# Kernel optimization log

Measured on AMD Instinct MI355X. Metric: run time of the kernel, lower is better.

The kernel has to match this reference:

```python
import jax, jax.numpy as jnp
import numpy as np

GROUPS = 32
EPS = 1e-5


def _group_norm(x, w, b):
    B, C, H, W = x.shape
    xr = x.reshape(B, GROUPS, C // GROUPS, H, W)
    mean = xr.mean(axis=(2, 3, 4), keepdims=True)
    var = xr.var(axis=(2, 3, 4), keepdims=True)
    xn = ((xr - mean) * jax.lax.rsqrt(var + EPS)).reshape(B, C, H, W)
    return xn * w[None, :, None, None] + b[None, :, None, None]


def _conv1x1(w, b, x):
    # 1x1 conv == per-pixel channel matmul
    return jnp.einsum('oc,bchw->bohw', w, x) + b[None, :, None, None]


def setup_inputs() -> dict:
    key = jax.random.key(0)
    ks = jax.random.split(key, 6)
    C = 512
    s = 1.0 / np.sqrt(C)  # kaiming-uniform-ish scale for 1x1 convs
    return {
        'x': jax.random.normal(ks[0], (4, C, 64, 64), jnp.float32),
        'gn_w': jnp.ones((C,), jnp.float32),
        'gn_b': jnp.zeros((C,), jnp.float32),
        'qw': jax.random.normal(ks[1], (C, C), jnp.float32) * s,
        'qb': jnp.zeros((C,), jnp.float32),
        'kw': jax.random.normal(ks[2], (C, C), jnp.float32) * s,
        'kb': jnp.zeros((C,), jnp.float32),
        'vw': jax.random.normal(ks[3], (C, C), jnp.float32) * s,
        'vb': jnp.zeros((C,), jnp.float32),
        'pw': jax.random.normal(ks[4], (C, C), jnp.float32) * s,
        'pb': jnp.zeros((C,), jnp.float32),
    }


def reference(x, gn_w, gn_b, qw, qb, kw, kb, vw, vb, pw, pb):
    B, C, H, W = x.shape
    h_ = _group_norm(x, gn_w, gn_b)
    q = _conv1x1(qw, qb, h_).reshape(B, C, H * W)
    k = _conv1x1(kw, kb, h_).reshape(B, C, H * W)
    v = _conv1x1(vw, vb, h_).reshape(B, C, H * W)
    # scores [B, HW(query), HW(key)]
    scores = jnp.einsum('bcq,bck->bqk', q, k) * (C ** -0.5)
    attn = jax.nn.softmax(scores, axis=-1)
    out = jnp.einsum('bqk,bdk->bdq', attn, v).reshape(B, C, H, W)
    return x + _conv1x1(pw, pb, out)
```

## Files before the change

### kernel.cpp

```cpp
#include <hip/hip_runtime.h>

#define DEV __device__ __forceinline__

typedef __attribute__((ext_vector_type(8))) short short8;
typedef __attribute__((ext_vector_type(4))) float floatx4;
typedef __attribute__((ext_vector_type(4))) int i32x4;
typedef __attribute__((ext_vector_type(2))) long longx2;

DEV unsigned short f2bs(float x) {
    unsigned u = __float_as_uint(x);
    unsigned r = (u + 0x7fffu + ((u >> 16) & 1u)) >> 16;
    return (unsigned short)r;
}

DEV unsigned char f2fp8(float x) {
#if __has_builtin(__builtin_amdgcn_cvt_pk_fp8_f32)
    int pk = __builtin_amdgcn_cvt_pk_fp8_f32(x, 0.f, 0, false);
    return (unsigned char)(pk & 0xff);
#else
    unsigned u = __float_as_uint(x);
    unsigned s = (u >> 24) & 0x80;
    unsigned a = u & 0x7fffffff;
    unsigned um = a + 0x7ffffu + ((a >> 20) & 1u);
    unsigned r = (a >= 0x3c800000u) ? ((um >> 20) - 0x3C0u) : 0u;
    return (unsigned char)(r | s);
#endif
}

DEV unsigned pack_fp8x4(float v0, float v1, float v2, float v3) {
#if __has_builtin(__builtin_amdgcn_cvt_pk_fp8_f32)
    unsigned pk = (unsigned)__builtin_amdgcn_cvt_pk_fp8_f32(v0, v1, 0, false);
    pk = (unsigned)__builtin_amdgcn_cvt_pk_fp8_f32(v2, v3, (int)pk, true);
    return pk;
#else
    return (unsigned)f2fp8(v0) | ((unsigned)f2fp8(v1) << 8) |
           ((unsigned)f2fp8(v2) << 16) | ((unsigned)f2fp8(v3) << 24);
#endif
}

DEV unsigned pack_i8x4(float v0, float v1, float v2, float v3) {
    unsigned b0 = (unsigned)((int)rintf(v0)) & 255u;
    unsigned b1 = (unsigned)((int)rintf(v1)) & 255u;
    unsigned b2 = (unsigned)((int)rintf(v2)) & 255u;
    unsigned b3 = (unsigned)((int)rintf(v3)) & 255u;
    return b0 | (b1 << 8) | (b2 << 16) | (b3 << 24);
}

DEV void syncfull() {
    asm volatile("s_waitcnt vmcnt(0) lgkmcnt(0)" ::: "memory");
    __builtin_amdgcn_sched_barrier(0);
    __builtin_amdgcn_s_barrier();
    __builtin_amdgcn_sched_barrier(0);
}

__global__ void pre_kernel(const float* __restrict__ x,
                           const float* __restrict__ qw, const float* __restrict__ kw,
                           const float* __restrict__ vw, const float* __restrict__ pw,
                           const float* __restrict__ qb, const float* __restrict__ kb,
                           unsigned short* __restrict__ wqkb, unsigned short* __restrict__ wvb,
                           unsigned short* __restrict__ wpb,
                           float* __restrict__ biasqk,
                           float* __restrict__ stats) {
    int b = blockIdx.x, tid = threadIdx.x;
    if (b < 768) {
        const float* src = (b < 256) ? qw : (b < 512) ? kw : vw;
        unsigned short* dst = (b < 256) ? wqkb : (b < 512) ? (wqkb + 262144) : wvb;
        int off = (b & 255) * 256 + tid;
        float4 v = ((const float4*)src)[off];
        ushort4 o;
        o.x = f2bs(v.x); o.y = f2bs(v.y); o.z = f2bs(v.z); o.w = f2bs(v.w);
        ((ushort4*)dst)[off] = o;
    } else if (b < 1024) {
        int off = (b - 768) * 256 + tid;
        int row = off >> 7, c4 = (off & 127) * 4;
        float4 v = ((const float4*)pw)[off];
        float vv[4] = {v.x, v.y, v.z, v.w};
#pragma unroll
        for (int e = 0; e < 4; ++e) {
            int c = c4 + e;
            int j = (c >> 4) & 3, lc = c & 15;
            int cp = (c & ~63) | (lc * 4 + j);
            wpb[row * 512 + cp] = f2bs(vv[e]);
        }
    } else if (b == 1024) {
        biasqk[tid]       = qb[tid];
        biasqk[256 + tid] = qb[256 + tid];
        biasqk[512 + tid] = kb[tid];
        biasqk[768 + tid] = kb[256 + tid];
    } else {
        int bg = b - 1025;
        const float4* p = (const float4*)(x + (size_t)bg * 65536);
        float s = 0.f, ss = 0.f;
        for (int i = tid; i < 16384; i += 256) {
            float4 v = p[i];
            s += v.x + v.y + v.z + v.w;
            ss += v.x * v.x + v.y * v.y + v.z * v.z + v.w * v.w;
        }
        for (int off = 32; off; off >>= 1) { s += __shfl_down(s, off); ss += __shfl_down(ss, off); }
        __shared__ float rs[4], rss[4];
        int wave = tid >> 6, lane = tid & 63;
        if (lane == 0) { rs[wave] = s; rss[wave] = ss; }
        __syncthreads();
        if (tid == 0) {
            float S = rs[0] + rs[1] + rs[2] + rs[3];
            float SS = rss[0] + rss[1] + rss[2] + rss[3];
            float mean = S * (1.f / 65536.f);
            float var = SS * (1.f / 65536.f) - mean * mean;
            stats[bg * 2] = mean;
            stats[bg * 2 + 1] = rsqrtf(var + 1e-5f);
        }
    }
}

__global__ void gn_apply_kernel(const float* __restrict__ x, const float* __restrict__ stats,
                                const float* __restrict__ gw, const float* __restrict__ gb,
                                unsigned short* __restrict__ ht) {
    __shared__ __align__(16) unsigned short t[64][72];
    int b = blockIdx.z, c0 = blockIdx.y * 64, p0 = blockIdx.x * 64;
    int tid = threadIdx.x;
    const float* xb = x + ((size_t)b * 512 + c0) * 4096 + p0;
#pragma unroll
    for (int pass = 0; pass < 4; ++pass) {
        int cl = pass * 16 + (tid >> 4);
        int pq = (tid & 15) * 4;
        float4 v = *(const float4*)(xb + (size_t)cl * 4096 + pq);
        int c = c0 + cl, g = c >> 4;
        float mean = stats[(b * 32 + g) * 2], rstd = stats[(b * 32 + g) * 2 + 1];
        float sw = gw[c] * rstd;
        float sb = gb[c] - mean * sw;
        t[pq + 0][cl] = f2bs(v.x * sw + sb);
        t[pq + 1][cl] = f2bs(v.y * sw + sb);
        t[pq + 2][cl] = f2bs(v.z * sw + sb);
        t[pq + 3][cl] = f2bs(v.w * sw + sb);
    }
    __syncthreads();
    unsigned short* hb = ht + ((size_t)b * 4096 + p0) * 512 + c0;
#pragma unroll
    for (int pass = 0; pass < 2; ++pass) {
        int pl = pass * 32 + (tid >> 3);
        int c8 = (tid & 7) * 8;
        *(uint4*)(hb + (size_t)pl * 512 + c8) = *(const uint4*)&t[pl][c8];
    }
}

__global__ void gemm_qkv(const unsigned short* __restrict__ h_t, long long sP,
                         const unsigned short* __restrict__ wqkb,
                         const unsigned short* __restrict__ wvb,
                         char* __restrict__ q_i8, char* __restrict__ k_i8,
                         char* __restrict__ v_f8,
                         const float* __restrict__ biasqk, const float* __restrict__ vb,
                         float qs) {
    __shared__ __align__(16) unsigned short lA[128 * 64];
    __shared__ __align__(16) unsigned short lB[128 * 64];
    const int tid = threadIdx.x;
    const int wave = tid >> 6, lane = tid & 63;
    const int flat = blockIdx.x;
    const bool isqk = flat < 1024;
    int m0, n0, bz;
    const unsigned short *Ab, *Bb;
    if (isqk) {
        m0 = ((flat >> 3) & 31) * 128;
        n0 = (flat & 7) * 128;
        bz = flat >> 8;
        Ab = h_t + (size_t)bz * sP;
        Bb = wqkb;
    } else {
        const int g = flat - 1024;
        m0 = ((g >> 5) & 3) * 128;
        n0 = (g & 31) * 128;
        bz = g >> 7;
        Ab = wvb;
        Bb = h_t + (size_t)bz * sP;
    }

    floatx4 acc[4][4];
#pragma unroll
    for (int i = 0; i < 4; i++)
#pragma unroll
        for (int j = 0; j < 4; j++) acc[i][j] = (floatx4){0.f, 0.f, 0.f, 0.f};

    const int wm = (wave >> 1) * 64, wn = (wave & 1) * 64;
    const int quad = lane >> 4;
    const int lc = lane & 15;
    const int lc7 = lc & 7;

    for (int kt = 0; kt < 8; ++kt) {
        const int kbase = kt * 64;
#pragma unroll
        for (int c = 0; c < 4; ++c) {
            int d = c * 256 + tid;
            int r = d >> 3;
            int kc = (d & 7) ^ (r & 7);
            const unsigned short* ga = Ab + (size_t)(m0 + r) * 512 + kbase + kc * 8;
            const unsigned short* gb = Bb + (size_t)(n0 + r) * 512 + kbase + kc * 8;
            __builtin_amdgcn_global_load_lds(
                (const __attribute__((address_space(1))) void*)ga,
                (__attribute__((address_space(3))) void*)&lA[(size_t)(c * 256 + wave * 64) * 8], 16, 0, 0);
            __builtin_amdgcn_global_load_lds(
                (const __attribute__((address_space(1))) void*)gb,
                (__attribute__((address_space(3))) void*)&lB[(size_t)(c * 256 + wave * 64) * 8], 16, 0, 0);
        }
        __syncthreads();
#pragma unroll
        for (int kk = 0; kk < 2; ++kk) {
            const int swz = ((kk * 4 + quad) ^ lc7) * 8;
            short8 af[4], bf[4];
#pragma unroll
            for (int i = 0; i < 4; i++)
                af[i] = *(const short8*)&lA[(size_t)(wm + i * 16 + lc) * 64 + swz];
#pragma unroll
            for (int j = 0; j < 4; j++)
                bf[j] = *(const short8*)&lB[(size_t)(wn + j * 16 + lc) * 64 + swz];
#pragma unroll
            for (int i = 0; i < 4; i++)
#pragma unroll
                for (int j = 0; j < 4; j++)
                    acc[i][j] = __builtin_amdgcn_mfma_f32_16x16x32_bf16(af[i], bf[j], acc[i][j], 0, 0, 0);
        }
        __syncthreads();
    }

    const int rowb = quad * 4;
    if (isqk) {
#pragma unroll
        for (int i = 0; i < 4; i++) {
#pragma unroll
            for (int r = 0; r < 4; r++) {
                const int m = m0 + wm + i * 16 + rowb + r;
                float q[4];
#pragma unroll
                for (int j = 0; j < 4; j++) {
                    const int n = n0 + wn + j * 16 + lc;
                    q[j] = fminf(fmaxf((acc[i][j][r] + biasqk[n]) * qs, -127.f), 127.f);
                }
                const int col64 = n0 + wn;
                char* outp = (col64 < 512) ? q_i8 : k_i8;
                size_t idx = (size_t)bz * sP + (size_t)m * 512 +
                             (col64 - ((col64 < 512) ? 0 : 512)) + lc * 4;
                *(unsigned*)(outp + idx) = pack_i8x4(q[0], q[1], q[2], q[3]);
            }
        }
    } else {
#pragma unroll
        for (int i = 0; i < 4; i++) {
#pragma unroll
            for (int r = 0; r < 4; r++) {
                const int m = m0 + wm + i * 16 + rowb + r;
                const float bm = vb[m];
                float q[4];
#pragma unroll
                for (int j = 0; j < 4; j++)
                    q[j] = fminf(fmaxf(acc[i][j][r] + bm, -448.f), 448.f);
                size_t idx = (size_t)bz * sP + (size_t)m * 4096 + n0 + wn + lc * 4;
                *(unsigned*)(v_f8 + idx) = pack_fp8x4(q[0], q[1], q[2], q[3]);
            }
        }
    }
}

__global__ __launch_bounds__(512, 2) void attn_fused(
    const char* __restrict__ Qg, const char* __restrict__ Kg,
    const char* __restrict__ Vg,
    unsigned short* __restrict__ Ou, long long sOb,
    float* __restrict__ rsum, float scale2) {
    __shared__ __align__(16) char Ql[128 * 512];
    __shared__ __align__(16) char Kl[64 * 512];
    __shared__ __align__(16) char Vl[512 * 64];
    __shared__ __align__(16) char Pl[128 * 64];
    const int tid = threadIdx.x;
    const int wave = tid >> 6, lane = tid & 63;
    const int quad = lane >> 4, lc = lane & 15;
    const int id = blockIdx.x;
    const int xcd = id & 7, qi = id >> 3;
    const int bz = xcd >> 1, split = xcd & 1;
    const int q0 = qi * 128;
    const int kvbase = split * 2048;
    const int NIT = 32;

    const char* Qb = Qg + ((size_t)bz * 4096 + q0) * 512;
    const char* Kb = Kg + ((size_t)bz * 4096 + kvbase) * 512;
    const char* Vb = Vg + (size_t)bz * 2097152 + kvbase;

    const int wq = wave * 16;
    const int mO = (wave >> 2) * 64, nO = (wave & 3) * 128;

    auto stageQ = [&]() {
#pragma unroll
        for (int c = 0; c < 8; ++c) {
            int f = c * 512 + tid;
            int r = f >> 5, g = f & 31;
            int gs = (g & 24) | ((g & 7) ^ (r & 7));
            __builtin_amdgcn_global_load_lds(
                (const __attribute__((address_space(1))) void*)(Qb + (size_t)r * 512 + gs * 16),
                (__attribute__((address_space(3))) void*)(Ql + (size_t)f * 16), 16, 0, 0);
        }
    };
    auto stageK = [&](int t) {
#pragma unroll
        for (int c = 0; c < 4; ++c) {
            int f = c * 512 + tid;
            int r = f >> 5, g = f & 31;
            int gs = (g & 24) | ((g & 7) ^ (r & 7));
            __builtin_amdgcn_global_load_lds(
                (const __attribute__((address_space(1))) void*)(Kb + (size_t)(t * 64 + r) * 512 + gs * 16),
                (__attribute__((address_space(3))) void*)(Kl + (size_t)f * 16), 16, 0, 0);
        }
    };
    auto stageV = [&](int t) {
#pragma unroll
        for (int c = 0; c < 4; ++c) {
            int f = c * 512 + tid;
            int r = f >> 2, g = f & 3;
            int gs = g ^ (r & 3);
            __builtin_amdgcn_global_load_lds(
                (const __attribute__((address_space(1))) void*)(Vb + (size_t)r * 4096 + t * 64 + gs * 16),
                (__attribute__((address_space(3))) void*)(Vl + (size_t)f * 16), 16, 0, 0);
        }
    };

    floatx4 acco[4][8];
#pragma unroll
    for (int i = 0; i < 4; ++i)
#pragma unroll
        for (int j = 0; j < 8; ++j) acco[i][j] = (floatx4){0.f, 0.f, 0.f, 0.f};
    float rs = 0.f;

    stageQ();
    stageK(0);
    stageV(0);
    syncfull();

    const int q = wq + lc;
    const int q7 = q & 7;

    for (int t = 0; t < NIT; ++t) {
        if (t > 0) stageV(t);
        i32x4 accs[4];
#pragma unroll
        for (int ki = 0; ki < 4; ++ki) accs[ki] = (i32x4){0, 0, 0, 0};
#pragma unroll
        for (int ks = 0; ks < 8; ++ks) {
            const int g = ks * 4 + quad;
            i32x4 bfrag = *(const i32x4*)&Ql[(size_t)q * 512 +
                                             (((g & 24) | ((g & 7) ^ q7)) << 4)];
#pragma unroll
            for (int ki = 0; ki < 4; ++ki) {
                const int ar = ki * 16 + lc;
                i32x4 afrag = *(const i32x4*)&Kl[(size_t)ar * 512 +
                                                 (((g & 24) | ((g & 7) ^ (ar & 7))) << 4)];
                accs[ki] = __builtin_amdgcn_mfma_i32_16x16x64_i8(afrag, bfrag, accs[ki], 0, 0, 0);
            }
        }
        float e[4][4];
#pragma unroll
        for (int ki = 0; ki < 4; ++ki)
#pragma unroll
            for (int r = 0; r < 4; ++r) {
                e[ki][r] = fminf(exp2f(fmaf((float)accs[ki][r], scale2, -2.0f)), 448.f);
                rs += e[ki][r];
            }
#pragma unroll
        for (int r = 0; r < 4; ++r) {
            unsigned w = pack_fp8x4(e[0][r], e[1][r], e[2][r], e[3][r]);
            const int s4 = quad * 4 + r;
            const int byte = q * 64 + (((s4 >> 1) ^ q7) << 3) + ((s4 & 1) << 2);
            *(unsigned*)&Pl[byte] = w;
        }
        syncfull();

        if (t + 1 < NIT) stageK(t + 1);
#pragma unroll
        for (int ks2 = 0; ks2 < 2; ++ks2) {
            long pa[4], vf[8];
#pragma unroll
            for (int i = 0; i < 4; ++i) {
                const int row = mO + i * 16 + lc;
                pa[i] = *(const long*)&Pl[(size_t)row * 64 +
                                          (((ks2 * 4 + quad) ^ (row & 7)) << 3)];
            }
#pragma unroll
            for (int j = 0; j < 8; ++j) {
                const int row = nO + j * 16 + lc;
                const int g16 = ks2 * 2 + (quad >> 1);
                vf[j] = *(const long*)&Vl[(size_t)row * 64 +
                                          ((g16 ^ (row & 3)) << 4) + ((quad & 1) << 3)];
            }
#pragma unroll
            for (int i = 0; i < 4; ++i)
#pragma unroll
                for (int j = 0; j < 8; ++j)
                    acco[i][j] = __builtin_amdgcn_mfma_f32_16x16x32_fp8_fp8(pa[i], vf[j], acco[i][j], 0, 0, 0);
        }
        syncfull();
    }

    rs += __shfl_xor(rs, 16);
    rs += __shfl_xor(rs, 32);
    if (quad == 0) rsum[((size_t)(split * 4 + bz)) * 4096 + q0 + q] = rs;

#pragma unroll
    for (int i = 0; i < 4; ++i) {
#pragma unroll
        for (int r = 0; r < 4; ++r) {
            const int m = q0 + mO + i * 16 + quad * 4 + r;
            unsigned short h[8];
#pragma unroll
            for (int j = 0; j < 8; ++j) h[j] = f2bs(acco[i][j][r]);
            unsigned short* base = Ou + (size_t)bz * sOb + (size_t)m * 1024 + split * 512 + nO;
            uint2 u0, u1;
            u0.x = (unsigned)h[0] | ((unsigned)h[1] << 16);
            u0.y = (unsigned)h[2] | ((unsigned)h[3] << 16);
            u1.x = (unsigned)h[4] | ((unsigned)h[5] << 16);
            u1.y = (unsigned)h[6] | ((unsigned)h[7] << 16);
            *(uint2*)(base + lc * 4) = u0;
            *(uint2*)(base + 64 + lc * 4) = u1;
        }
    }
}

__global__ void gemm_proj(const unsigned short* __restrict__ A,
                          const unsigned short* __restrict__ B, long long sBb,
                          float* __restrict__ Cv, long long sCb,
                          const float* __restrict__ bias,
                          const float* __restrict__ resid, long long sRb,
                          const float* __restrict__ rsum,
                          int M, int N, int K) {
    __shared__ __align__(16) unsigned short lA[128 * 64];
    __shared__ __align__(16) unsigned short lB[128 * 64];
    const int tid = threadIdx.x;
    const int wave = tid >> 6, lane = tid & 63;
    const int m0 = blockIdx.y * 128, n0 = blockIdx.x * 128, bz = blockIdx.z;
    const unsigned short* Ab = A;
    const unsigned short* Bb = B + (size_t)bz * sBb;

    floatx4 acc[4][4];
#pragma unroll
    for (int i = 0; i < 4; i++)
#pragma unroll
        for (int j = 0; j < 4; j++) acc[i][j] = (floatx4){0.f, 0.f, 0.f, 0.f};

    const int wm = (wave >> 1) * 64, wn = (wave & 1) * 64;
    const int quad = lane >> 4;
    const int lc = lane & 15;
    const int lc7 = lc & 7;

    const int nk = K >> 6;
    for (int kt = 0; kt < nk; ++kt) {
        const int kbase = kt * 64;
#pragma unroll
        for (int c = 0; c < 4; ++c) {
            int d = c * 256 + tid;
            int r = d >> 3;
            int kc = (d & 7) ^ (r & 7);
            const unsigned short* ga = Ab + (size_t)(m0 + r) * 512 + ((kbase & 511) + kc * 8);
            const unsigned short* gb = Bb + (size_t)(n0 + r) * 1024 + kbase + kc * 8;
            __builtin_amdgcn_global_load_lds(
                (const __attribute__((address_space(1))) void*)ga,
                (__attribute__((address_space(3))) void*)&lA[(size_t)(c * 256 + wave * 64) * 8], 16, 0, 0);
            __builtin_amdgcn_global_load_lds(
                (const __attribute__((address_space(1))) void*)gb,
                (__attribute__((address_space(3))) void*)&lB[(size_t)(c * 256 + wave * 64) * 8], 16, 0, 0);
        }
        __syncthreads();
#pragma unroll
        for (int kk = 0; kk < 2; ++kk) {
            const int swz = ((kk * 4 + quad) ^ lc7) * 8;
            short8 af[4], bf[4];
#pragma unroll
            for (int i = 0; i < 4; i++)
                af[i] = *(const short8*)&lA[(size_t)(wm + i * 16 + lc) * 64 + swz];
#pragma unroll
            for (int j = 0; j < 4; j++)
                bf[j] = *(const short8*)&lB[(size_t)(wn + j * 16 + lc) * 64 + swz];
#pragma unroll
            for (int i = 0; i < 4; i++)
#pragma unroll
                for (int j = 0; j < 4; j++)
                    acc[i][j] = __builtin_amdgcn_mfma_f32_16x16x32_bf16(af[i], bf[j], acc[i][j], 0, 0, 0);
        }
        __syncthreads();
    }

    float rsinv[4];
#pragma unroll
    for (int j = 0; j < 4; j++) {
        const int n = n0 + wn + j * 16 + lc;
        rsinv[j] = 1.f / (rsum[(size_t)bz * 4096 + n] + rsum[(size_t)(4 + bz) * 4096 + n]);
    }

    const int rowb = quad * 4;
#pragma unroll
    for (int i = 0; i < 4; i++) {
#pragma unroll
        for (int r = 0; r < 4; r++) {
            const int m = m0 + wm + i * 16 + rowb + r;
            const float bm = bias[m];
#pragma unroll
            for (int j = 0; j < 4; j++) {
                const int n = n0 + wn + j * 16 + lc;
                size_t idx = (size_t)bz * sCb + (size_t)m * N + n;
                Cv[idx] = acc[i][j][r] * rsinv[j] + bm + resid[(size_t)bz * sRb + (size_t)m * N + n];
            }
        }
    }
}

extern "C" void kernel_launch(void* const* d_in, const int* in_sizes, int n_in,
                              void* d_out, int out_size, void* d_ws, size_t ws_size,
                              hipStream_t stream) {
    (void)in_sizes; (void)n_in; (void)out_size; (void)ws_size;
    const float* x   = (const float*)d_in[0];
    const float* gnw = (const float*)d_in[1];
    const float* gnb = (const float*)d_in[2];
    const float* qw  = (const float*)d_in[3];
    const float* qb  = (const float*)d_in[4];
    const float* kw  = (const float*)d_in[5];
    const float* kb  = (const float*)d_in[6];
    const float* vw  = (const float*)d_in[7];
    const float* vb  = (const float*)d_in[8];
    const float* pw  = (const float*)d_in[9];
    const float* pb  = (const float*)d_in[10];
    float* out = (float*)d_out;

    char* ws = (char*)d_ws;
    unsigned short* h_t = (unsigned short*)(ws);
    char* q_i8 = (char*)(ws + (16ull << 20));
    char* k_i8 = (char*)(ws + (32ull << 20));
    char* v_f8 = (char*)(ws + (48ull << 20));
    unsigned short* wqkb = (unsigned short*)(ws + (64ull << 20));
    unsigned short* wvb = (unsigned short*)(ws + (65ull << 20));
    unsigned short* wpb = wvb + 262144;
    float* stats  = (float*)(ws + (66ull << 20));
    float* biasqk = (float*)(ws + (66ull << 20) + 8192);
    float* rowsum = (float*)(ws + (66ull << 20) + 65536);
    unsigned short* o_un = (unsigned short*)(ws + (72ull << 20));

    const long long sP  = 2097152;
    const long long sOb = 4194304;
    const float QS = 16.f;
    const float SC = 0.044194173824159216f / (QS * QS);
    const float LOG2E = 1.4426950408889634f;

    pre_kernel<<<1153, 256, 0, stream>>>(x, qw, kw, vw, pw, qb, kb, wqkb, wvb, wpb,
                                         biasqk, stats);
    gn_apply_kernel<<<dim3(64, 8, 4), 256, 0, stream>>>(x, stats, gnw, gnb, h_t);
    gemm_qkv<<<1536, 256, 0, stream>>>(h_t, sP, wqkb, wvb, q_i8, k_i8, v_f8, biasqk, vb, QS);
    attn_fused<<<dim3(256), 512, 0, stream>>>(q_i8, k_i8, v_f8, o_un, sOb, rowsum,
                                              SC * LOG2E);
    gemm_proj<<<dim3(32, 4, 4), 256, 0, stream>>>(wpb, o_un, sOb, out, sP, pb, x, sP,
                                                  rowsum, 512, 4096, 1024);
}
```

Baseline: 313.6 us.

## Re-layout attention LDS tiles for wide 16-byte fragment reads

Rewrites the shared-memory layouts of Q, K, V and P in the fused attention kernel. Q and K are stored in 128-byte channel chunks with XOR swizzle, and V is packed two channel rows per 128-byte LDS row. P uses an 80-byte padded row stride so the PV stage reads 16-byte fragments, halving the number of LDS reads, and issues the MFMAs in two passes over the pair. The goal is fewer LDS instructions and fewer bank conflicts in the inner loop. It adds complex index mapping that could introduce conflicts or correctness risk if the swizzles mismatch.

```diff
diff --git a/kernel.cpp b/kernel.cpp
--- a/kernel.cpp
+++ b/kernel.cpp
@@ -258,166 +258,6 @@
     }
 }
 
-__global__ __launch_bounds__(512, 2) void attn_fused(
-    const char* __restrict__ Qg, const char* __restrict__ Kg,
-    const char* __restrict__ Vg,
-    unsigned short* __restrict__ Ou, long long sOb,
-    float* __restrict__ rsum, float scale2) {
-    __shared__ __align__(16) char Ql[128 * 512];
-    __shared__ __align__(16) char Kl[64 * 512];
-    __shared__ __align__(16) char Vl[512 * 64];
-    __shared__ __align__(16) char Pl[128 * 64];
-    const int tid = threadIdx.x;
-    const int wave = tid >> 6, lane = tid & 63;
-    const int quad = lane >> 4, lc = lane & 15;
-    const int id = blockIdx.x;
-    const int xcd = id & 7, qi = id >> 3;
-    const int bz = xcd >> 1, split = xcd & 1;
-    const int q0 = qi * 128;
-    const int kvbase = split * 2048;
-    const int NIT = 32;
-
-    const char* Qb = Qg + ((size_t)bz * 4096 + q0) * 512;
-    const char* Kb = Kg + ((size_t)bz * 4096 + kvbase) * 512;
-    const char* Vb = Vg + (size_t)bz * 2097152 + kvbase;
-
-    const int wq = wave * 16;
-    const int mO = (wave >> 2) * 64, nO = (wave & 3) * 128;
-
-    auto stageQ = [&]() {
-#pragma unroll
-        for (int c = 0; c < 8; ++c) {
-            int f = c * 512 + tid;
-            int r = f >> 5, g = f & 31;
-            int gs = (g & 24) | ((g & 7) ^ (r & 7));
-            __builtin_amdgcn_global_load_lds(
-                (const __attribute__((address_space(1))) void*)(Qb + (size_t)r * 512 + gs * 16),
-                (__attribute__((address_space(3))) void*)(Ql + (size_t)f * 16), 16, 0, 0);
-        }
-    };
-    auto stageK = [&](int t) {
-#pragma unroll
-        for (int c = 0; c < 4; ++c) {
-            int f = c * 512 + tid;
-            int r = f >> 5, g = f & 31;
-            int gs = (g & 24) | ((g & 7) ^ (r & 7));
-            __builtin_amdgcn_global_load_lds(
-                (const __attribute__((address_space(1))) void*)(Kb + (size_t)(t * 64 + r) * 512 + gs * 16),
-                (__attribute__((address_space(3))) void*)(Kl + (size_t)f * 16), 16, 0, 0);
-        }
-    };
-    auto stageV = [&](int t) {
-#pragma unroll
-        for (int c = 0; c < 4; ++c) {
-            int f = c * 512 + tid;
-            int r = f >> 2, g = f & 3;
-            int gs = g ^ (r & 3);
-            __builtin_amdgcn_global_load_lds(
-                (const __attribute__((address_space(1))) void*)(Vb + (size_t)r * 4096 + t * 64 + gs * 16),
-                (__attribute__((address_space(3))) void*)(Vl + (size_t)f * 16), 16, 0, 0);
-        }
-    };
-
-    floatx4 acco[4][8];
-#pragma unroll
-    for (int i = 0; i < 4; ++i)
-#pragma unroll
-        for (int j = 0; j < 8; ++j) acco[i][j] = (floatx4){0.f, 0.f, 0.f, 0.f};
-    float rs = 0.f;
-
-    stageQ();
-    stageK(0);
-    stageV(0);
-    syncfull();
-
-    const int q = wq + lc;
-    const int q7 = q & 7;
-
-    for (int t = 0; t < NIT; ++t) {
-        if (t > 0) stageV(t);
-        i32x4 accs[4];
-#pragma unroll
-        for (int ki = 0; ki < 4; ++ki) accs[ki] = (i32x4){0, 0, 0, 0};
-#pragma unroll
-        for (int ks = 0; ks < 8; ++ks) {
-            const int g = ks * 4 + quad;
-            i32x4 bfrag = *(const i32x4*)&Ql[(size_t)q * 512 +
-                                             (((g & 24) | ((g & 7) ^ q7)) << 4)];
-#pragma unroll
-            for (int ki = 0; ki < 4; ++ki) {
-                const int ar = ki * 16 + lc;
-                i32x4 afrag = *(const i32x4*)&Kl[(size_t)ar * 512 +
-                                                 (((g & 24) | ((g & 7) ^ (ar & 7))) << 4)];
-                accs[ki] = __builtin_amdgcn_mfma_i32_16x16x64_i8(afrag, bfrag, accs[ki], 0, 0, 0);
-            }
-        }
-        float e[4][4];
-#pragma unroll
-        for (int ki = 0; ki < 4; ++ki)
-#pragma unroll
-            for (int r = 0; r < 4; ++r) {
-                e[ki][r] = fminf(exp2f(fmaf((float)accs[ki][r], scale2, -2.0f)), 448.f);
-                rs += e[ki][r];
-            }
-#pragma unroll
-        for (int r = 0; r < 4; ++r) {
-            unsigned w = pack_fp8x4(e[0][r], e[1][r], e[2][r], e[3][r]);
-            const int s4 = quad * 4 + r;
-            const int byte = q * 64 + (((s4 >> 1) ^ q7) << 3) + ((s4 & 1) << 2);
-            *(unsigned*)&Pl[byte] = w;
-        }
-        syncfull();
-
-        if (t + 1 < NIT) stageK(t + 1);
-#pragma unroll
-        for (int ks2 = 0; ks2 < 2; ++ks2) {
-            long pa[4], vf[8];
-#pragma unroll
-            for (int i = 0; i < 4; ++i) {
-                const int row = mO + i * 16 + lc;
-                pa[i] = *(const long*)&Pl[(size_t)row * 64 +
-                                          (((ks2 * 4 + quad) ^ (row & 7)) << 3)];
-            }
-#pragma unroll
-            for (int j = 0; j < 8; ++j) {
-                const int row = nO + j * 16 + lc;
-                const int g16 = ks2 * 2 + (quad >> 1);
-                vf[j] = *(const long*)&Vl[(size_t)row * 64 +
-                                          ((g16 ^ (row & 3)) << 4) + ((quad & 1) << 3)];
-            }
-#pragma unroll
-            for (int i = 0; i < 4; ++i)
-#pragma unroll
-                for (int j = 0; j < 8; ++j)
-                    acco[i][j] = __builtin_amdgcn_mfma_f32_16x16x32_fp8_fp8(pa[i], vf[j], acco[i][j], 0, 0, 0);
-        }
-        syncfull();
-    }
-
-    rs += __shfl_xor(rs, 16);
-    rs += __shfl_xor(rs, 32);
-    if (quad == 0) rsum[((size_t)(split * 4 + bz)) * 4096 + q0 + q] = rs;
-
-#pragma unroll
-    for (int i = 0; i < 4; ++i) {
-#pragma unroll
-        for (int r = 0; r < 4; ++r) {
-            const int m = q0 + mO + i * 16 + quad * 4 + r;
-            unsigned short h[8];
-#pragma unroll
-            for (int j = 0; j < 8; ++j) h[j] = f2bs(acco[i][j][r]);
-            unsigned short* base = Ou + (size_t)bz * sOb + (size_t)m * 1024 + split * 512 + nO;
-            uint2 u0, u1;
-            u0.x = (unsigned)h[0] | ((unsigned)h[1] << 16);
-            u0.y = (unsigned)h[2] | ((unsigned)h[3] << 16);
-            u1.x = (unsigned)h[4] | ((unsigned)h[5] << 16);
-            u1.y = (unsigned)h[6] | ((unsigned)h[7] << 16);
-            *(uint2*)(base + lc * 4) = u0;
-            *(uint2*)(base + 64 + lc * 4) = u1;
-        }
-    }
-}
-
 __global__ void gemm_proj(const unsigned short* __restrict__ A,
                           const unsigned short* __restrict__ B, long long sBb,
                           float* __restrict__ Cv, long long sCb,
@@ -501,6 +341,175 @@
                 size_t idx = (size_t)bz * sCb + (size_t)m * N + n;
                 Cv[idx] = acc[i][j][r] * rsinv[j] + bm + resid[(size_t)bz * sRb + (size_t)m * N + n];
             }
+        }
+    }
+}
+
+__global__ __launch_bounds__(512, 2) void attn_fused(
+    const char* __restrict__ Qg, const char* __restrict__ Kg,
+    const char* __restrict__ Vg,
+    unsigned short* __restrict__ Ou, long long sOb,
+    float* __restrict__ rsum, float scale2) {
+    __shared__ __align__(16) char Ql[512 * 128];
+    __shared__ __align__(16) char Kl[256 * 128];
+    __shared__ __align__(16) char Vl[256 * 128];
+    __shared__ __align__(16) char Pl[128 * 80];
+    const int tid = threadIdx.x;
+    const int wave = tid >> 6, lane = tid & 63;
+    const int quad = lane >> 4, lc = lane & 15;
+    const int lc7 = lc & 7;
+    const int id = blockIdx.x;
+    const int xcd = id & 7, qi = id >> 3;
+    const int bz = xcd >> 1, split = xcd & 1;
+    const int q0 = qi * 128;
+    const int kvbase = split * 2048;
+    const int NIT = 32;
+
+    const char* Qb = Qg + ((size_t)bz * 4096 + q0) * 512;
+    const char* Kb = Kg + ((size_t)bz * 4096 + kvbase) * 512;
+    const char* Vb = Vg + (size_t)bz * 2097152 + kvbase;
+
+    const int wq = wave * 16;
+    const int mO = (wave >> 2) * 64, nO = (wave & 3) * 128;
+
+    auto stageQ = [&]() {
+#pragma unroll
+        for (int c = 0; c < 8; ++c) {
+            int f = c * 512 + tid;
+            int rr = f >> 3, cs = f & 7;
+            int qq = rr & 127, chq = rr >> 7;
+            int s = cs ^ (qq & 7);
+            __builtin_amdgcn_global_load_lds(
+                (const __attribute__((address_space(1))) void*)(Qb + (size_t)qq * 512 + chq * 128 + s * 16),
+                (__attribute__((address_space(3))) void*)(Ql + (size_t)f * 16), 16, 0, 0);
+        }
+    };
+    auto stageK = [&](int t) {
+#pragma unroll
+        for (int c = 0; c < 4; ++c) {
+            int f = c * 512 + tid;
+            int rr = f >> 3, cs = f & 7;
+            int kv = rr & 63, chq = rr >> 6;
+            int s = cs ^ (kv & 7);
+            __builtin_amdgcn_global_load_lds(
+                (const __attribute__((address_space(1))) void*)(Kb + (size_t)(t * 64 + kv) * 512 + chq * 128 + s * 16),
+                (__attribute__((address_space(3))) void*)(Kl + (size_t)f * 16), 16, 0, 0);
+        }
+    };
+    auto stageV = [&](int t) {
+#pragma unroll
+        for (int c = 0; c < 4; ++c) {
+            int f = c * 512 + tid;
+            int rr = f >> 3, cs = f & 7;
+            int cp = cs ^ (rr & 7);
+            int d = rr + ((cp >> 2) << 8);
+            int gq = cp & 3;
+            __builtin_amdgcn_global_load_lds(
+                (const __attribute__((address_space(1))) void*)(Vb + (size_t)d * 4096 + t * 64 + gq * 16),
+                (__attribute__((address_space(3))) void*)(Vl + (size_t)f * 16), 16, 0, 0);
+        }
+    };
+
+    floatx4 acco[4][8];
+#pragma unroll
+    for (int i = 0; i < 4; ++i)
+#pragma unroll
+        for (int j = 0; j < 8; ++j) acco[i][j] = (floatx4){0.f, 0.f, 0.f, 0.f};
+    float rs = 0.f;
+
+    stageQ();
+    stageK(0);
+    stageV(0);
+    syncfull();
+
+    const int q = wq + lc;
+    const int q7 = q & 7;
+
+    for (int t = 0; t < NIT; ++t) {
+        if (t > 0) stageV(t);
+        i32x4 accs[4];
+#pragma unroll
+        for (int ki = 0; ki < 4; ++ki) accs[ki] = (i32x4){0, 0, 0, 0};
+#pragma unroll
+        for (int ks = 0; ks < 8; ++ks) {
+            const int g = ks * 4 + quad;
+            const int gh = g >> 3, gl = g & 7;
+            i32x4 bfrag = *(const i32x4*)&Ql[(size_t)(gh * 128 + q) * 128 + ((gl ^ q7) << 4)];
+#pragma unroll
+            for (int ki = 0; ki < 4; ++ki) {
+                const int ar = ki * 16 + lc;
+                i32x4 afrag = *(const i32x4*)&Kl[(size_t)(gh * 64 + ar) * 128 + ((gl ^ lc7) << 4)];
+                accs[ki] = __builtin_amdgcn_mfma_i32_16x16x64_i8(afrag, bfrag, accs[ki], 0, 0, 0);
+            }
+        }
+        float e[4][4];
+#pragma unroll
+        for (int ki = 0; ki < 4; ++ki)
+#pragma unroll
+            for (int r = 0; r < 4; ++r) {
+                e[ki][r] = fminf(exp2f(fmaf((float)accs[ki][r], scale2, -2.0f)), 448.f);
+                rs += e[ki][r];
+            }
+        {
+            unsigned w0 = pack_fp8x4(e[0][0], e[1][0], e[2][0], e[3][0]);
+            unsigned w1 = pack_fp8x4(e[0][1], e[1][1], e[2][1], e[3][1]);
+            unsigned w2 = pack_fp8x4(e[0][2], e[1][2], e[2][2], e[3][2]);
+            unsigned w3 = pack_fp8x4(e[0][3], e[1][3], e[2][3], e[3][3]);
+            uint2 s0; s0.x = w0; s0.y = w1;
+            uint2 s1; s1.x = w2; s1.y = w3;
+            *(uint2*)&Pl[(size_t)q * 80 + quad * 16 + 0] = s0;
+            *(uint2*)&Pl[(size_t)q * 80 + quad * 16 + 8] = s1;
+        }
+        syncfull();
+
+        if (t + 1 < NIT) stageK(t + 1);
+        {
+            longx2 pv[4], vv[8];
+#pragma unroll
+            for (int i = 0; i < 4; ++i) {
+                const int row = mO + i * 16 + lc;
+                pv[i] = *(const longx2*)&Pl[(size_t)row * 80 + quad * 16];
+            }
+#pragma unroll
+            for (int j = 0; j < 8; ++j) {
+                const int row = nO + j * 16 + lc;
+                const int r8 = row & 255, hi = row >> 8;
+                vv[j] = *(const longx2*)&Vl[(size_t)r8 * 128 + (((hi << 2) + quad) ^ lc7) * 16];
+            }
+#pragma unroll
+            for (int i = 0; i < 4; ++i)
+#pragma unroll
+                for (int j = 0; j < 8; ++j)
+                    acco[i][j] = __builtin_amdgcn_mfma_f32_16x16x32_fp8_fp8(pv[i][0], vv[j][0], acco[i][j], 0, 0, 0);
+#pragma unroll
+            for (int i = 0; i < 4; ++i)
+#pragma unroll
+                for (int j = 0; j < 8; ++j)
+                    acco[i][j] = __builtin_amdgcn_mfma_f32_16x16x32_fp8_fp8(pv[i][1], vv[j][1], acco[i][j], 0, 0, 0);
+        }
+        syncfull();
+    }
+
+    rs += __shfl_xor(rs, 16);
+    rs += __shfl_xor(rs, 32);
+    if (quad == 0) rsum[((size_t)(split * 4 + bz)) * 4096 + q0 + q] = rs;
+
+#pragma unroll
+    for (int i = 0; i < 4; ++i) {
+#pragma unroll
+        for (int r = 0; r < 4; ++r) {
+            const int m = q0 + mO + i * 16 + quad * 4 + r;
+            unsigned short h[8];
+#pragma unroll
+            for (int j = 0; j < 8; ++j) h[j] = f2bs(acco[i][j][r]);
+            unsigned short* base = Ou + (size_t)bz * sOb + (size_t)m * 1024 + split * 512 + nO;
+            uint2 u0, u1;
+            u0.x = (unsigned)h[0] | ((unsigned)h[1] << 16);
+            u0.y = (unsigned)h[2] | ((unsigned)h[3] << 16);
+            u1.x = (unsigned)h[4] | ((unsigned)h[5] << 16);
+            u1.y = (unsigned)h[6] | ((unsigned)h[7] << 16);
+            *(uint2*)(base + lc * 4) = u0;
+            *(uint2*)(base + 64 + lc * 4) = u1;
         }
     }
 }
```

After: 291.3 us. 7.1% less time.
